# Kernel optimization log

Measured on AMD Instinct MI355X. Metric: run time of the kernel, lower is better.

The kernel has to match this reference:

```python
import jax, jax.numpy as jnp
import numpy as np

WH, WW = 8, 8            # window size
N = WH * WW              # tokens per window = 64
DIM = 512
HEADS = 16
NW = 64                  # windows per image (mask batch)
B = 1024                 # total windows = 16 images * 64 windows
CPB_HIDDEN = 512


def _make_buffers():
    # relative coords table for CPB-MLP: [1, 2*WH-1, 2*WW-1, 2]
    rch = np.arange(-(WH - 1), WH, dtype=np.float32)
    rcw = np.arange(-(WW - 1), WW, dtype=np.float32)
    table = np.stack(np.meshgrid(rch, rcw, indexing='ij'), axis=-1)[None]
    table[..., 0] /= (WH - 1)
    table[..., 1] /= (WW - 1)
    table *= 8.0
    table = np.sign(table) * np.log2(np.abs(table) + 1.0) / 3.0
    # relative position index: [N, N]
    coords = np.stack(np.meshgrid(np.arange(WH), np.arange(WW), indexing='ij'), 0).reshape(2, -1)
    rel = coords[:, :, None] - coords[:, None, :]      # [2, N, N]
    rel = rel.transpose(1, 2, 0).astype(np.int64)
    rel[..., 0] += WH - 1
    rel[..., 1] += WW - 1
    rel[..., 0] *= 2 * WW - 1
    idx = rel.sum(-1)
    return jnp.asarray(table, jnp.float32), jnp.asarray(idx, jnp.int32)


def setup_inputs() -> dict:
    key = jax.random.key(0)
    ks = jax.random.split(key, 8)
    table, idx = _make_buffers()
    return {
        'x': jax.random.normal(ks[0], (B, N, DIM), jnp.float32),
        'mask': jax.random.normal(ks[1], (NW, N, N), jnp.float32),
        'qkv_w': jax.random.normal(ks[2], (3 * DIM, DIM), jnp.float32) * 0.02,
        'q_bias': jnp.zeros((DIM,), jnp.float32),
        'v_bias': jnp.zeros((DIM,), jnp.float32),
        'logit_scale': jnp.full((HEADS, 1, 1), np.log(10.0), jnp.float32),
        'cpb_w1': jax.random.normal(ks[3], (CPB_HIDDEN, 2), jnp.float32) * 0.02,
        'cpb_b1': jnp.zeros((CPB_HIDDEN,), jnp.float32),
        'cpb_w2': jax.random.normal(ks[4], (HEADS, CPB_HIDDEN), jnp.float32) * 0.02,
        'proj_w': jax.random.normal(ks[5], (DIM, DIM), jnp.float32) * 0.02,
        'proj_b': jnp.zeros((DIM,), jnp.float32),
        'rel_coords_table': table,
        'rel_pos_index': idx,
    }


def _l2norm(t):
    n = jnp.sqrt(jnp.sum(t * t, axis=-1, keepdims=True))
    return t / jnp.maximum(n, 1e-12)


def reference(x, mask, qkv_w, q_bias, v_bias, logit_scale, cpb_w1, cpb_b1,
              cpb_w2, proj_w, proj_b, rel_coords_table, rel_pos_index):
    Bq, Nq, C = x.shape
    qkv_b = jnp.concatenate([q_bias, jnp.zeros_like(v_bias), v_bias])
    qkv = x @ qkv_w.T + qkv_b                                  # [B, N, 3C]
    qkv = qkv.reshape(Bq, Nq, 3, HEADS, C // HEADS).transpose(2, 0, 3, 1, 4)
    q, k, v = qkv[0], qkv[1], qkv[2]                           # [B, H, N, D]
    attn = jnp.einsum('bhnd,bhmd->bhnm', _l2norm(q), _l2norm(k))
    scale = jnp.exp(jnp.minimum(logit_scale, jnp.log(jnp.float32(100.0))))
    attn = attn * scale                                        # [B, H, N, N]
    # CPB-MLP relative position bias
    hidden = jax.nn.relu(rel_coords_table @ cpb_w1.T + cpb_b1)  # [1, 2WH-1, 2WW-1, 512]
    bias_table = (hidden @ cpb_w2.T).reshape(-1, HEADS)         # [(2WH-1)(2WW-1), H]
    rel_bias = bias_table[rel_pos_index.reshape(-1)].reshape(Nq, Nq, HEADS)
    rel_bias = 16.0 * jax.nn.sigmoid(rel_bias.transpose(2, 0, 1))  # [H, N, N]
    attn = attn + rel_bias[None]
    nW = mask.shape[0]
    attn = attn.reshape(Bq // nW, nW, HEADS, Nq, Nq) + mask[None, :, None]
    attn = jax.nn.softmax(attn.reshape(Bq, HEADS, Nq, Nq), axis=-1)
    out = jnp.einsum('bhnm,bhmd->bhnd', attn, v)
    out = out.transpose(0, 2, 1, 3).reshape(Bq, Nq, C)
    return out @ proj_w.T + proj_b
```

## Files before the change

### kernel.cpp

```cpp
#include <hip/hip_runtime.h>
#include <hip/hip_bf16.h>

typedef __bf16 bf16;
typedef __bf16 bf16x4 __attribute__((ext_vector_type(4)));
typedef __bf16 bf16x8 __attribute__((ext_vector_type(8)));
typedef float floatx4 __attribute__((ext_vector_type(4)));

#define MFMA16(a, b, c) __builtin_amdgcn_mfma_f32_16x16x32_bf16((a), (b), (c), 0, 0, 0)

static constexpr long OFF_QKV   = 0;
static constexpr long OFF_XB    = 201326592;
static constexpr long OFF_WQKV  = 268435456;
static constexpr long OFF_WPROJ = 270008320;
static constexpr long OFF_BT    = 270532608;
static constexpr long OFF_RB    = 270548992;

__device__ __forceinline__ void load_lds16(const bf16* g, bf16* l) {
  __builtin_amdgcn_global_load_lds((const __attribute__((address_space(1))) void*)(g),
                                   (__attribute__((address_space(3))) void*)(l), 16, 0, 0);
}

__global__ __launch_bounds__(256) void cvt_f32_bf16(const float* __restrict__ src,
                                                    bf16* __restrict__ dst, int n8) {
  int i = blockIdx.x * 256 + threadIdx.x;
  if (i < n8) {
    const float4* s = (const float4*)src;
    float4 a = s[2 * i], b = s[2 * i + 1];
    bf16x8 o;
    o[0] = (bf16)a.x; o[1] = (bf16)a.y; o[2] = (bf16)a.z; o[3] = (bf16)a.w;
    o[4] = (bf16)b.x; o[5] = (bf16)b.y; o[6] = (bf16)b.z; o[7] = (bf16)b.w;
    ((bf16x8*)dst)[i] = o;
  }
}

__global__ __launch_bounds__(256) void cpb_mlp(const float* __restrict__ table,
                                               const float* __restrict__ w1,
                                               const float* __restrict__ b1,
                                               const float* __restrict__ w2,
                                               float* __restrict__ bias_table) {
  __shared__ float hid[512];
  const int e = blockIdx.x;
  const float t0 = table[e * 2 + 0], t1 = table[e * 2 + 1];
  for (int j = threadIdx.x; j < 512; j += 256) {
    float hv = t0 * w1[j * 2 + 0] + t1 * w1[j * 2 + 1] + b1[j];
    hid[j] = hv > 0.f ? hv : 0.f;
  }
  __syncthreads();
  const int hd = threadIdx.x >> 4, l = threadIdx.x & 15;
  float p = 0.f;
  for (int j = l; j < 512; j += 16) p += hid[j] * w2[hd * 512 + j];
  #pragma unroll
  for (int d = 8; d >= 1; d >>= 1) p += __shfl_xor(p, d, 16);
  if (l == 0) bias_table[e * 16 + hd] = p;
}

__global__ __launch_bounds__(256) void cpb_gather(const float* __restrict__ bias_table,
                                                  const int* __restrict__ idx,
                                                  float* __restrict__ rel_bias) {
  int f = blockIdx.x * 256 + threadIdx.x;
  int h = f >> 12, ij = f & 4095;
  float v = bias_table[idx[ij] * 16 + h];
  rel_bias[f] = 16.f / (1.f + __expf(-v));
}

template <int NN, bool QKV>
__global__ __launch_bounds__(512, 2) void gemm_bt(const bf16* __restrict__ A,
                                                  const bf16* __restrict__ Bt,
                                                  void* __restrict__ outv,
                                                  const float* __restrict__ bias_a,
                                                  const float* __restrict__ bias_b) {
  constexpr int K = 512;
  constexpr int nblk = NN / 256;
  __shared__ alignas(16) bf16 As[4][8192];
  __shared__ alignas(16) bf16 Bs[4][8192];
  const int tid = threadIdx.x;
  const int lane = tid & 63;
  const int wv = tid >> 6;
  const int bid = blockIdx.x;
  const int xcd = bid & 7;
  const int g = bid >> 3;
  const int mb = xcd * 32 + g / nblk;
  const int nb = g % nblk;
  const long m0 = (long)mb * 256;
  const int n0 = nb * 256;
  const int wm = (wv >> 2) * 128;
  const int wn = (wv & 3) * 64;
  const int cl = lane & 15;
  const int cq = lane >> 4;
  const int wbase = tid & ~63;
  const int sx = (cq ^ ((cl >> 1) & 3)) << 3;

  const floatx4 fzero = {0.f, 0.f, 0.f, 0.f};
  floatx4 acc[8][4];
  #pragma unroll
  for (int i = 0; i < 8; ++i)
    #pragma unroll
    for (int j = 0; j < 4; ++j) acc[i][j] = fzero;

  auto stageA = [&](int kh) {
    #pragma unroll
    for (int o = 0; o < 2; ++o) {
      const int s = o * 512 + tid;
      const int r = s >> 2;
      const int gl = (s & 3) ^ ((s >> 3) & 3);
      const bf16* ga = A + (m0 + r) * (long)K + kh * 32 + gl * 8;
      load_lds16(ga, &As[kh & 3][(o * 512 + wbase) * 8]);
    }
  };
  auto stageB = [&](int kh) {
    #pragma unroll
    for (int o = 0; o < 2; ++o) {
      const int s = o * 512 + tid;
      const int r = s >> 2;
      const int gl = (s & 3) ^ ((s >> 3) & 3);
      const bf16* gb = Bt + (long)(n0 + r) * K + kh * 32 + gl * 8;
      load_lds16(gb, &Bs[kh & 3][(o * 512 + wbase) * 8]);
    }
  };

  auto kstep = [&](int h, int slot, bool doStage, int vmN, bool lastH) {
    if (doStage) { stageA(h + 3); stageB(h + 3); }
    bf16x8 bfr[4], af[8];
    #pragma unroll
    for (int n = 0; n < 4; ++n) {
      const int r = wn + n * 16 + cl;
      bfr[n] = *(const bf16x8*)&Bs[slot][r * 32 + sx];
    }
    #pragma unroll
    for (int m = 0; m < 8; ++m) {
      const int r = wm + m * 16 + cl;
      af[m] = *(const bf16x8*)&As[slot][r * 32 + sx];
    }
    __builtin_amdgcn_s_setprio(1);
    #pragma unroll
    for (int i = 0; i < 8; ++i)
      #pragma unroll
      for (int j = 0; j < 4; ++j)
        acc[i][j] = MFMA16(bfr[j], af[i], acc[i][j]);
    __builtin_amdgcn_s_setprio(0);
    __builtin_amdgcn_sched_barrier(0);
    if (vmN == 8)      asm volatile("s_waitcnt vmcnt(8)" ::: "memory");
    else if (vmN == 4) asm volatile("s_waitcnt vmcnt(4)" ::: "memory");
    else if (vmN == 0) asm volatile("s_waitcnt vmcnt(0)" ::: "memory");
    if (!lastH) __builtin_amdgcn_s_barrier();
  };

  stageA(0); stageB(0); stageA(1); stageB(1); stageA(2); stageB(2);
  asm volatile("s_waitcnt vmcnt(8)" ::: "memory");
  __builtin_amdgcn_s_barrier();

  #pragma unroll 4
  for (int h = 0; h < 12; ++h) kstep(h, h & 3, true, 8, false);
  kstep(12, 0, true, 8, false);
  kstep(13, 1, false, 4, false);
  kstep(14, 2, false, 0, false);
  kstep(15, 3, false, -1, true);

  const int cq4 = cq * 4;
  #pragma unroll
  for (int i = 0; i < 8; ++i) {
    const long m = m0 + wm + i * 16 + cl;
    #pragma unroll
    for (int j = 0; j < 4; ++j) {
      const int nbase = n0 + wn + j * 16 + cq4;
      if constexpr (QKV) {
        float4 bb = {0.f, 0.f, 0.f, 0.f};
        if (nbase < 512) bb = *(const float4*)&bias_a[nbase];
        else if (nbase >= 1024) bb = *(const float4*)&bias_b[nbase - 1024];
        bf16x4 o;
        o[0] = (bf16)(acc[i][j][0] + bb.x);
        o[1] = (bf16)(acc[i][j][1] + bb.y);
        o[2] = (bf16)(acc[i][j][2] + bb.z);
        o[3] = (bf16)(acc[i][j][3] + bb.w);
        *(bf16x4*)((bf16*)outv + m * NN + nbase) = o;
      } else {
        const float4 bb = *(const float4*)&bias_a[nbase];
        float4 o;
        o.x = acc[i][j][0] + bb.x;
        o.y = acc[i][j][1] + bb.y;
        o.z = acc[i][j][2] + bb.z;
        o.w = acc[i][j][3] + bb.w;
        *(float4*)((float*)outv + m * NN + nbase) = o;
      }
    }
  }
}

__global__ __launch_bounds__(256, 5) void attn_kernel(const bf16* __restrict__ qkv,
                                                      const float* __restrict__ mask,
                                                      const float* __restrict__ lscale,
                                                      const float* __restrict__ rel_bias,
                                                      bf16* __restrict__ out) {
  const int bid = blockIdx.x;
  const int xcd = bid & 7;
  const int t = bid >> 3;
  const int p = xcd + ((t >> 1) << 3);
  const int b = p >> 3;
  const int h = ((p & 7) << 1) | (t & 1);
  const int wi = b & 63;
  const int tid = threadIdx.x;
  const int lane = tid & 63;
  const int wv = tid >> 6;
  const int cl = lane & 15;
  const int cq = lane >> 4;

  __shared__ alignas(16) bf16 smem[12544];
  bf16* qh_s = smem;
  bf16* ql_s = smem + 2560;
  bf16* kh_s = smem + 5120;
  bf16* kl_s = smem + 7680;
  bf16* vT   = smem + 10240;
  bf16* ps   = smem;

  {
    const int r = tid >> 2, seg = tid & 3;
    const bf16* base = qkv + (long)(b * 64 + r) * 1536 + h * 32 + seg * 8;
    float f[8], ss;
    bf16x8 hi, lo;

    bf16x8 qv = *(const bf16x8*)(base);
    ss = 0.f;
    #pragma unroll
    for (int j = 0; j < 8; ++j) { f[j] = (float)qv[j]; ss += f[j] * f[j]; }
    ss += __shfl_xor(ss, 1, 4); ss += __shfl_xor(ss, 2, 4);
    float s1 = 1.f / fmaxf(sqrtf(ss), 1e-12f);
    #pragma unroll
    for (int j = 0; j < 8; ++j) {
      float xn = f[j] * s1;
      bf16 xh = (bf16)xn;
      hi[j] = xh; lo[j] = (bf16)(xn - (float)xh);
    }
    *(bf16x8*)&qh_s[r * 40 + seg * 8] = hi;
    *(bf16x8*)&ql_s[r * 40 + seg * 8] = lo;

    bf16x8 kv = *(const bf16x8*)(base + 512);
    ss = 0.f;
    #pragma unroll
    for (int j = 0; j < 8; ++j) { f[j] = (float)kv[j]; ss += f[j] * f[j]; }
    ss += __shfl_xor(ss, 1, 4); ss += __shfl_xor(ss, 2, 4);
    s1 = 1.f / fmaxf(sqrtf(ss), 1e-12f);
    #pragma unroll
    for (int j = 0; j < 8; ++j) {
      float xn = f[j] * s1;
      bf16 xh = (bf16)xn;
      hi[j] = xh; lo[j] = (bf16)(xn - (float)xh);
    }
    *(bf16x8*)&kh_s[r * 40 + seg * 8] = hi;
    *(bf16x8*)&kl_s[r * 40 + seg * 8] = lo;

    bf16x8 vv = *(const bf16x8*)(base + 1024);
    #pragma unroll
    for (int j = 0; j < 8; ++j) vT[(seg * 8 + j) * 72 + r] = vv[j];
  }
  __syncthreads();

  const float sc = __expf(fminf(lscale[h], 4.6051701859880914f));

  const int mrow = wv * 16 + cl;
  const bf16x8 aqh = *(const bf16x8*)&qh_s[mrow * 40 + cq * 8];
  const bf16x8 aql = *(const bf16x8*)&ql_s[mrow * 40 + cq * 8];
  floatx4 sacc[4];
  #pragma unroll
  for (int nt = 0; nt < 4; ++nt) {
    const int nr = nt * 16 + cl;
    const bf16x8 bkh = *(const bf16x8*)&kh_s[nr * 40 + cq * 8];
    const bf16x8 bkl = *(const bf16x8*)&kl_s[nr * 40 + cq * 8];
    floatx4 a = {0.f, 0.f, 0.f, 0.f};
    a = MFMA16(aql, bkh, a);
    a = MFMA16(aqh, bkl, a);
    a = MFMA16(aqh, bkh, a);
    sacc[nt] = a;
  }
  __syncthreads();

  float pw[4][4];
  #pragma unroll
  for (int rg = 0; rg < 4; ++rg) {
    const int row = wv * 16 + cq * 4 + rg;
    const float* rbp = rel_bias + h * 4096 + row * 64;
    const float* mkp = mask + wi * 4096 + row * 64;
    float mxv = -1e30f;
    #pragma unroll
    for (int nt = 0; nt < 4; ++nt) {
      float s = sacc[nt][rg] * sc + rbp[nt * 16 + cl] + mkp[nt * 16 + cl];
      pw[rg][nt] = s;
      mxv = fmaxf(mxv, s);
    }
    #pragma unroll
    for (int d = 8; d >= 1; d >>= 1) mxv = fmaxf(mxv, __shfl_xor(mxv, d, 16));
    float sm = 0.f;
    #pragma unroll
    for (int nt = 0; nt < 4; ++nt) {
      float e = __expf(pw[rg][nt] - mxv);
      pw[rg][nt] = e;
      sm += e;
    }
    #pragma unroll
    for (int d = 8; d >= 1; d >>= 1) sm += __shfl_xor(sm, d, 16);
    const float inv = 1.f / sm;
    #pragma unroll
    for (int nt = 0; nt < 4; ++nt)
      ps[row * 72 + nt * 16 + cl] = (bf16)(pw[rg][nt] * inv);
  }

  floatx4 oacc[2];
  oacc[0] = (floatx4){0.f, 0.f, 0.f, 0.f};
  oacc[1] = (floatx4){0.f, 0.f, 0.f, 0.f};
  #pragma unroll
  for (int ks = 0; ks < 2; ++ks) {
    const bf16x8 ap = *(const bf16x8*)&ps[(wv * 16 + cl) * 72 + ks * 32 + cq * 8];
    #pragma unroll
    for (int nt = 0; nt < 2; ++nt) {
      const bf16x8 bv = *(const bf16x8*)&vT[(nt * 16 + cl) * 72 + ks * 32 + cq * 8];
      oacc[nt] = MFMA16(bv, ap, oacc[nt]);
    }
  }
  const long obase = (long)(b * 64 + wv * 16 + cl) * 512 + h * 32 + cq * 4;
  #pragma unroll
  for (int nt = 0; nt < 2; ++nt) {
    bf16x4 o;
    #pragma unroll
    for (int r = 0; r < 4; ++r) o[r] = (bf16)oacc[nt][r];
    *(bf16x4*)&out[obase + nt * 16] = o;
  }
}

extern "C" void kernel_launch(void* const* d_in, const int* in_sizes, int n_in,
                              void* d_out, int out_size, void* d_ws, size_t ws_size,
                              hipStream_t stream) {
  const float* x      = (const float*)d_in[0];
  const float* mask   = (const float*)d_in[1];
  const float* qkv_w  = (const float*)d_in[2];
  const float* q_bias = (const float*)d_in[3];
  const float* v_bias = (const float*)d_in[4];
  const float* lsc    = (const float*)d_in[5];
  const float* cpb_w1 = (const float*)d_in[6];
  const float* cpb_b1 = (const float*)d_in[7];
  const float* cpb_w2 = (const float*)d_in[8];
  const float* proj_w = (const float*)d_in[9];
  const float* proj_b = (const float*)d_in[10];
  const float* table  = (const float*)d_in[11];
  const int*   relidx = (const int*)d_in[12];

  char* ws = (char*)d_ws;
  bf16* qkvb   = (bf16*)(ws + OFF_QKV);
  bf16* xb     = (bf16*)(ws + OFF_XB);
  bf16* wqkv   = (bf16*)(ws + OFF_WQKV);
  bf16* wproj  = (bf16*)(ws + OFF_WPROJ);
  float* btab  = (float*)(ws + OFF_BT);
  float* rbias = (float*)(ws + OFF_RB);

  cvt_f32_bf16<<<16384, 256, 0, stream>>>(x, xb, 65536 * 512 / 8);
  cvt_f32_bf16<<<384, 256, 0, stream>>>(qkv_w, wqkv, 1536 * 512 / 8);
  cvt_f32_bf16<<<128, 256, 0, stream>>>(proj_w, wproj, 512 * 512 / 8);
  cpb_mlp<<<225, 256, 0, stream>>>(table, cpb_w1, cpb_b1, cpb_w2, btab);
  cpb_gather<<<256, 256, 0, stream>>>(btab, relidx, rbias);

  gemm_bt<1536, true><<<1536, 512, 0, stream>>>(xb, wqkv, (void*)qkvb, q_bias, v_bias);
  attn_kernel<<<16384, 256, 0, stream>>>(qkvb, mask, lsc, rbias, xb);
  gemm_bt<512, false><<<512, 512, 0, stream>>>(xb, wproj, d_out, proj_b, nullptr);
}
```

Before: 540.1 us.

## Fuse fp32-to-bf16 conversion of x into QKV GEMM A-tile loads

The separate conversion kernel that turned the full fp32 input x into bf16 is removed. The QKV GEMM now loads fp32 A tiles into registers one k-step ahead, converts them to bf16 and writes them to LDS, avoiding the extra full-size write and re-read of the activation buffer. The k-loop for both GEMMs is also restructured into two half-tile MFMA phases with extra barriers, and B staging moves after the first phase. In exchange, the QKV GEMM reads twice as many A bytes per tile, re-read across the N-blocks, and loses asynchronous direct-to-LDS loads for A.

```diff
diff --git a/kernel.cpp b/kernel.cpp
--- a/kernel.cpp
+++ b/kernel.cpp
@@ -64,13 +64,15 @@
 }
 
 template <int NN, bool QKV>
-__global__ __launch_bounds__(512, 2) void gemm_bt(const bf16* __restrict__ A,
+__global__ __launch_bounds__(512, 2) void gemm_bt(const void* __restrict__ Ain,
                                                   const bf16* __restrict__ Bt,
                                                   void* __restrict__ outv,
                                                   const float* __restrict__ bias_a,
                                                   const float* __restrict__ bias_b) {
   constexpr int K = 512;
   constexpr int nblk = NN / 256;
+  const float* Af = (const float*)Ain;
+  const bf16*  Ab = (const bf16*)Ain;
   __shared__ alignas(16) bf16 As[4][8192];
   __shared__ alignas(16) bf16 Bs[4][8192];
   const int tid = threadIdx.x;
@@ -97,64 +99,106 @@
     #pragma unroll
     for (int j = 0; j < 4; ++j) acc[i][j] = fzero;
 
-  auto stageA = [&](int kh) {
-    #pragma unroll
-    for (int o = 0; o < 2; ++o) {
-      const int s = o * 512 + tid;
-      const int r = s >> 2;
-      const int gl = (s & 3) ^ ((s >> 3) & 3);
-      const bf16* ga = A + (m0 + r) * (long)K + kh * 32 + gl * 8;
-      load_lds16(ga, &As[kh & 3][(o * 512 + wbase) * 8]);
-    }
+  const int rp0 = tid >> 2;
+  const int rp1 = rp0 + 128;
+  const int gl0 = (tid & 3) ^ ((tid >> 3) & 3);
+
+  auto stageB = [&](int j) {
+    const bf16* gb0 = Bt + (long)(n0 + rp0) * K + j * 32 + gl0 * 8;
+    load_lds16(gb0, &Bs[j & 3][wbase * 8]);
+    const bf16* gb1 = Bt + (long)(n0 + rp1) * K + j * 32 + gl0 * 8;
+    load_lds16(gb1, &Bs[j & 3][(512 + wbase) * 8]);
   };
-  auto stageB = [&](int kh) {
-    #pragma unroll
-    for (int o = 0; o < 2; ++o) {
-      const int s = o * 512 + tid;
-      const int r = s >> 2;
-      const int gl = (s & 3) ^ ((s >> 3) & 3);
-      const bf16* gb = Bt + (long)(n0 + r) * K + kh * 32 + gl * 8;
-      load_lds16(gb, &Bs[kh & 3][(o * 512 + wbase) * 8]);
-    }
+  auto stageA_gl = [&](int j) {
+    const bf16* ga0 = Ab + (m0 + rp0) * (long)K + j * 32 + gl0 * 8;
+    load_lds16(ga0, &As[j & 3][wbase * 8]);
+    const bf16* ga1 = Ab + (m0 + rp1) * (long)K + j * 32 + gl0 * 8;
+    load_lds16(ga1, &As[j & 3][(512 + wbase) * 8]);
   };
 
-  auto kstep = [&](int h, int slot, bool doStage, int vmN, bool lastH) {
-    if (doStage) { stageA(h + 3); stageB(h + 3); }
-    bf16x8 bfr[4], af[8];
-    #pragma unroll
-    for (int n = 0; n < 4; ++n) {
-      const int r = wn + n * 16 + cl;
-      bfr[n] = *(const bf16x8*)&Bs[slot][r * 32 + sx];
-    }
-    #pragma unroll
-    for (int m = 0; m < 8; ++m) {
-      const int r = wm + m * 16 + cl;
-      af[m] = *(const bf16x8*)&As[slot][r * 32 + sx];
-    }
+  float4 a0, a1, a2, a3;
+  auto issueA = [&](int j) {
+    const float4* s0 = (const float4*)(Af + (m0 + rp0) * (long)K + j * 32 + gl0 * 8);
+    const float4* s1 = (const float4*)(Af + (m0 + rp1) * (long)K + j * 32 + gl0 * 8);
+    a0 = s0[0]; a1 = s0[1]; a2 = s1[0]; a3 = s1[1];
+  };
+  auto writeA = [&](int j) {
+    bf16x8 v0, v1;
+    v0[0] = (bf16)a0.x; v0[1] = (bf16)a0.y; v0[2] = (bf16)a0.z; v0[3] = (bf16)a0.w;
+    v0[4] = (bf16)a1.x; v0[5] = (bf16)a1.y; v0[6] = (bf16)a1.z; v0[7] = (bf16)a1.w;
+    v1[0] = (bf16)a2.x; v1[1] = (bf16)a2.y; v1[2] = (bf16)a2.z; v1[3] = (bf16)a2.w;
+    v1[4] = (bf16)a3.x; v1[5] = (bf16)a3.y; v1[6] = (bf16)a3.z; v1[7] = (bf16)a3.w;
+    *(bf16x8*)&As[j & 3][tid * 8] = v0;
+    *(bf16x8*)&As[j & 3][(512 + tid) * 8] = v1;
+  };
+
+  if constexpr (QKV) {
+    issueA(0);
+    stageB(0); stageB(1); stageB(2);
+    writeA(0);
+    asm volatile("s_waitcnt vmcnt(4)" ::: "memory");
+    asm volatile("s_waitcnt lgkmcnt(0)" ::: "memory");
+  } else {
+    stageA_gl(0); stageB(0); stageA_gl(1); stageB(1); stageA_gl(2); stageB(2);
+    asm volatile("s_waitcnt vmcnt(8)" ::: "memory");
+  }
+  __builtin_amdgcn_s_barrier();
+
+  #pragma unroll
+  for (int h = 0; h < 16; ++h) {
+    const int slot = h & 3;
+    if constexpr (QKV) {
+      if (h + 1 <= 15) issueA(h + 1);
+    } else {
+      if (h + 3 <= 15) stageA_gl(h + 3);
+    }
+    bf16x8 af0[4], bfr[4];
+    #pragma unroll
+    for (int m = 0; m < 4; ++m)
+      af0[m] = *(const bf16x8*)&As[slot][(wm + m * 16 + cl) * 32 + sx];
+    #pragma unroll
+    for (int n = 0; n < 4; ++n)
+      bfr[n] = *(const bf16x8*)&Bs[slot][(wn + n * 16 + cl) * 32 + sx];
+    __builtin_amdgcn_s_barrier();
+    asm volatile("s_waitcnt lgkmcnt(0)" ::: "memory");
+    __builtin_amdgcn_sched_barrier(0);
     __builtin_amdgcn_s_setprio(1);
     #pragma unroll
-    for (int i = 0; i < 8; ++i)
+    for (int i = 0; i < 4; ++i)
       #pragma unroll
       for (int j = 0; j < 4; ++j)
-        acc[i][j] = MFMA16(bfr[j], af[i], acc[i][j]);
+        acc[i][j] = MFMA16(bfr[j], af0[i], acc[i][j]);
     __builtin_amdgcn_s_setprio(0);
+    __builtin_amdgcn_s_barrier();
     __builtin_amdgcn_sched_barrier(0);
-    if (vmN == 8)      asm volatile("s_waitcnt vmcnt(8)" ::: "memory");
-    else if (vmN == 4) asm volatile("s_waitcnt vmcnt(4)" ::: "memory");
-    else if (vmN == 0) asm volatile("s_waitcnt vmcnt(0)" ::: "memory");
-    if (!lastH) __builtin_amdgcn_s_barrier();
-  };
-
-  stageA(0); stageB(0); stageA(1); stageB(1); stageA(2); stageB(2);
-  asm volatile("s_waitcnt vmcnt(8)" ::: "memory");
-  __builtin_amdgcn_s_barrier();
-
-  #pragma unroll 4
-  for (int h = 0; h < 12; ++h) kstep(h, h & 3, true, 8, false);
-  kstep(12, 0, true, 8, false);
-  kstep(13, 1, false, 4, false);
-  kstep(14, 2, false, 0, false);
-  kstep(15, 3, false, -1, true);
+    if (h + 3 <= 15) stageB(h + 3);
+    if constexpr (QKV) {
+      if (h <= 12) asm volatile("s_waitcnt vmcnt(2)" ::: "memory");
+      if (h + 1 <= 15) writeA(h + 1);
+    } else {
+      if (h <= 12)      asm volatile("s_waitcnt vmcnt(8)" ::: "memory");
+      else if (h == 13) asm volatile("s_waitcnt vmcnt(4)" ::: "memory");
+      else if (h == 14) asm volatile("s_waitcnt vmcnt(0)" ::: "memory");
+    }
+    bf16x8 af1[4];
+    #pragma unroll
+    for (int m = 0; m < 4; ++m)
+      af1[m] = *(const bf16x8*)&As[slot][(wm + 64 + m * 16 + cl) * 32 + sx];
+    asm volatile("s_waitcnt lgkmcnt(0)" ::: "memory");
+    __builtin_amdgcn_s_barrier();
+    __builtin_amdgcn_sched_barrier(0);
+    __builtin_amdgcn_s_setprio(1);
+    #pragma unroll
+    for (int i = 0; i < 4; ++i)
+      #pragma unroll
+      for (int j = 0; j < 4; ++j)
+        acc[4 + i][j] = MFMA16(bfr[j], af1[i], acc[4 + i][j]);
+    __builtin_amdgcn_s_setprio(0);
+    if (h < 15) {
+      __builtin_amdgcn_s_barrier();
+      __builtin_amdgcn_sched_barrier(0);
+    }
+  }
 
   const int cq4 = cq * 4;
   #pragma unroll
@@ -350,13 +394,14 @@
   float* btab  = (float*)(ws + OFF_BT);
   float* rbias = (float*)(ws + OFF_RB);
 
-  cvt_f32_bf16<<<16384, 256, 0, stream>>>(x, xb, 65536 * 512 / 8);
   cvt_f32_bf16<<<384, 256, 0, stream>>>(qkv_w, wqkv, 1536 * 512 / 8);
   cvt_f32_bf16<<<128, 256, 0, stream>>>(proj_w, wproj, 512 * 512 / 8);
   cpb_mlp<<<225, 256, 0, stream>>>(table, cpb_w1, cpb_b1, cpb_w2, btab);
   cpb_gather<<<256, 256, 0, stream>>>(btab, relidx, rbias);
 
-  gemm_bt<1536, true><<<1536, 512, 0, stream>>>(xb, wqkv, (void*)qkvb, q_bias, v_bias);
+  gemm_bt<1536, true><<<1536, 512, 0, stream>>>((const void*)x, wqkv, (void*)qkvb,
+                                                q_bias, v_bias);
   attn_kernel<<<16384, 256, 0, stream>>>(qkvb, mask, lsc, rbias, xb);
-  gemm_bt<512, false><<<512, 512, 0, stream>>>(xb, wproj, d_out, proj_b, nullptr);
-}
+  gemm_bt<512, false><<<512, 512, 0, stream>>>((const void*)xb, wproj, d_out,
+                                               proj_b, nullptr);
+}
```

New measurement: 587.6 us. 1.09x slower.

## Add smaller-tile projection GEMM and transpose attention score MFMA for vectorized softmax

Applied to the files above, without the earlier changes.

The output projection gets its own kernel with 128x128 tiles, 256 threads, and a 3-slot LDS pipeline. This launches 2048 blocks instead of 512 so more CUs stay busy on the small N=512 GEMM. In attention, the QK^T MFMA operands are swapped so each lane holds one query row's scores. The softmax can then load bias and mask as float4, reduce with two cross-lane shuffles instead of four per row, and write probabilities as bf16x4. The smaller tiles lower data reuse per block.

```diff
diff --git a/kernel.cpp b/kernel.cpp
--- a/kernel.cpp
+++ b/kernel.cpp
@@ -63,13 +63,13 @@
   rel_bias[f] = 16.f / (1.f + __expf(-v));
 }
 
-template <int NN, bool QKV>
-__global__ __launch_bounds__(512, 2) void gemm_bt(const bf16* __restrict__ A,
-                                                  const bf16* __restrict__ Bt,
-                                                  void* __restrict__ outv,
-                                                  const float* __restrict__ bias_a,
-                                                  const float* __restrict__ bias_b) {
+__global__ __launch_bounds__(512, 2) void gemm_qkv(const bf16* __restrict__ A,
+                                                   const bf16* __restrict__ Bt,
+                                                   bf16* __restrict__ out,
+                                                   const float* __restrict__ bias_a,
+                                                   const float* __restrict__ bias_b) {
   constexpr int K = 512;
+  constexpr int NN = 1536;
   constexpr int nblk = NN / 256;
   __shared__ alignas(16) bf16 As[4][8192];
   __shared__ alignas(16) bf16 Bs[4][8192];
@@ -122,15 +122,11 @@
     if (doStage) { stageA(h + 3); stageB(h + 3); }
     bf16x8 bfr[4], af[8];
     #pragma unroll
-    for (int n = 0; n < 4; ++n) {
-      const int r = wn + n * 16 + cl;
-      bfr[n] = *(const bf16x8*)&Bs[slot][r * 32 + sx];
-    }
-    #pragma unroll
-    for (int m = 0; m < 8; ++m) {
-      const int r = wm + m * 16 + cl;
-      af[m] = *(const bf16x8*)&As[slot][r * 32 + sx];
-    }
+    for (int n = 0; n < 4; ++n)
+      bfr[n] = *(const bf16x8*)&Bs[slot][(wn + n * 16 + cl) * 32 + sx];
+    #pragma unroll
+    for (int m = 0; m < 8; ++m)
+      af[m] = *(const bf16x8*)&As[slot][(wm + m * 16 + cl) * 32 + sx];
     __builtin_amdgcn_s_setprio(1);
     #pragma unroll
     for (int i = 0; i < 8; ++i)
@@ -163,25 +159,115 @@
     #pragma unroll
     for (int j = 0; j < 4; ++j) {
       const int nbase = n0 + wn + j * 16 + cq4;
-      if constexpr (QKV) {
-        float4 bb = {0.f, 0.f, 0.f, 0.f};
-        if (nbase < 512) bb = *(const float4*)&bias_a[nbase];
-        else if (nbase >= 1024) bb = *(const float4*)&bias_b[nbase - 1024];
-        bf16x4 o;
-        o[0] = (bf16)(acc[i][j][0] + bb.x);
-        o[1] = (bf16)(acc[i][j][1] + bb.y);
-        o[2] = (bf16)(acc[i][j][2] + bb.z);
-        o[3] = (bf16)(acc[i][j][3] + bb.w);
-        *(bf16x4*)((bf16*)outv + m * NN + nbase) = o;
-      } else {
-        const float4 bb = *(const float4*)&bias_a[nbase];
-        float4 o;
-        o.x = acc[i][j][0] + bb.x;
-        o.y = acc[i][j][1] + bb.y;
-        o.z = acc[i][j][2] + bb.z;
-        o.w = acc[i][j][3] + bb.w;
-        *(float4*)((float*)outv + m * NN + nbase) = o;
-      }
+      float4 bb = {0.f, 0.f, 0.f, 0.f};
+      if (nbase < 512) bb = *(const float4*)&bias_a[nbase];
+      else if (nbase >= 1024) bb = *(const float4*)&bias_b[nbase - 1024];
+      bf16x4 o;
+      o[0] = (bf16)(acc[i][j][0] + bb.x);
+      o[1] = (bf16)(acc[i][j][1] + bb.y);
+      o[2] = (bf16)(acc[i][j][2] + bb.z);
+      o[3] = (bf16)(acc[i][j][3] + bb.w);
+      *(bf16x4*)(out + m * NN + nbase) = o;
+    }
+  }
+}
+
+__global__ __launch_bounds__(256, 4) void gemm_proj(const bf16* __restrict__ A,
+                                                    const bf16* __restrict__ Bt,
+                                                    float* __restrict__ outv,
+                                                    const float* __restrict__ bias_a) {
+  constexpr int K = 512;
+  constexpr int KT = K / 32;
+  constexpr int NN = 512;
+  constexpr int nblk = NN / 128;
+  __shared__ alignas(16) bf16 As[3][128 * 32];
+  __shared__ alignas(16) bf16 Bs[3][128 * 32];
+  const int tid = threadIdx.x;
+  const int lane = tid & 63;
+  const int wv = tid >> 6;
+  const int bid = blockIdx.x;
+  const int xcd = bid & 7;
+  const int g = bid >> 3;
+  const int mb = xcd * 64 + g / nblk;
+  const int nb = g % nblk;
+  const long m0 = (long)mb * 128;
+  const int n0 = nb * 128;
+  const int wm = (wv & 1) * 64;
+  const int wn = (wv >> 1) * 64;
+  const int cl = lane & 15;
+  const int cq = lane >> 4;
+  const int wbase = tid & ~63;
+
+  const floatx4 fzero = {0.f, 0.f, 0.f, 0.f};
+  floatx4 acc[4][4];
+  #pragma unroll
+  for (int i = 0; i < 4; ++i)
+    #pragma unroll
+    for (int j = 0; j < 4; ++j) acc[i][j] = fzero;
+
+  int srow[2], sgl[2];
+  #pragma unroll
+  for (int r = 0; r < 2; ++r) {
+    const int s = r * 256 + tid;
+    srow[r] = s >> 2;
+    sgl[r] = (s & 3) ^ ((s >> 3) & 3);
+  }
+  const int sx = cq ^ ((cl >> 1) & 3);
+
+  auto stage = [&](int slot, int j) {
+    const int k0 = j * 32;
+    #pragma unroll
+    for (int r = 0; r < 2; ++r) {
+      const bf16* ga = A + (m0 + srow[r]) * (long)K + (k0 + sgl[r] * 8);
+      load_lds16(ga, &As[slot][(r * 256 + wbase) * 8]);
+      const bf16* gb = Bt + (long)(n0 + srow[r]) * K + (k0 + sgl[r] * 8);
+      load_lds16(gb, &Bs[slot][(r * 256 + wbase) * 8]);
+    }
+  };
+
+  stage(0, 0);
+  stage(1, 1);
+  asm volatile("s_waitcnt vmcnt(4)" ::: "memory");
+  __builtin_amdgcn_s_barrier();
+
+  #pragma unroll
+  for (int h = 0; h < KT; ++h) {
+    const int slot = h % 3;
+    if (h + 2 < KT) stage((h + 2) % 3, h + 2);
+    bf16x8 af[4], bfr[4];
+    #pragma unroll
+    for (int t = 0; t < 4; ++t) {
+      af[t] = *(const bf16x8*)&As[slot][((wm + t * 16 + cl) * 4 + sx) * 8];
+      bfr[t] = *(const bf16x8*)&Bs[slot][((wn + t * 16 + cl) * 4 + sx) * 8];
+    }
+    __builtin_amdgcn_s_setprio(1);
+    #pragma unroll
+    for (int i = 0; i < 4; ++i)
+      #pragma unroll
+      for (int j = 0; j < 4; ++j)
+        acc[i][j] = MFMA16(bfr[j], af[i], acc[i][j]);
+    __builtin_amdgcn_s_setprio(0);
+    if (h <= KT - 3)
+      asm volatile("s_waitcnt vmcnt(4)" ::: "memory");
+    else if (h == KT - 2)
+      asm volatile("s_waitcnt vmcnt(0)" ::: "memory");
+    if (h + 1 < KT) __builtin_amdgcn_s_barrier();
+  }
+
+  const int cq4 = cq * 4;
+  #pragma unroll
+  for (int i = 0; i < 4; ++i) {
+    const long m = m0 + wm + i * 16 + cl;
+    #pragma unroll
+    for (int j = 0; j < 4; ++j) {
+      const int nbase = n0 + wn + j * 16 + cq4;
+      const float4 bb = *(const float4*)&bias_a[nbase];
+      float4 o;
+      o.x = acc[i][j][0] + bb.x;
+      o.y = acc[i][j][1] + bb.y;
+      o.z = acc[i][j][2] + bb.z;
+      o.w = acc[i][j][3] + bb.w;
+      *(float4*)(outv + m * NN + nbase) = o;
     }
   }
 }
@@ -256,9 +342,9 @@
 
   const float sc = __expf(fminf(lscale[h], 4.6051701859880914f));
 
-  const int mrow = wv * 16 + cl;
-  const bf16x8 aqh = *(const bf16x8*)&qh_s[mrow * 40 + cq * 8];
-  const bf16x8 aql = *(const bf16x8*)&ql_s[mrow * 40 + cq * 8];
+  const int row = wv * 16 + cl;
+  const bf16x8 aqh = *(const bf16x8*)&qh_s[row * 40 + cq * 8];
+  const bf16x8 aql = *(const bf16x8*)&ql_s[row * 40 + cq * 8];
   floatx4 sacc[4];
   #pragma unroll
   for (int nt = 0; nt < 4; ++nt) {
@@ -266,41 +352,52 @@
     const bf16x8 bkh = *(const bf16x8*)&kh_s[nr * 40 + cq * 8];
     const bf16x8 bkl = *(const bf16x8*)&kl_s[nr * 40 + cq * 8];
     floatx4 a = {0.f, 0.f, 0.f, 0.f};
-    a = MFMA16(aql, bkh, a);
-    a = MFMA16(aqh, bkl, a);
-    a = MFMA16(aqh, bkh, a);
+    a = MFMA16(bkh, aql, a);
+    a = MFMA16(bkl, aqh, a);
+    a = MFMA16(bkh, aqh, a);
     sacc[nt] = a;
   }
+
+  const float* rbp = rel_bias + h * 4096 + row * 64 + cq * 4;
+  const float* mkp = mask + wi * 4096 + row * 64 + cq * 4;
+  floatx4 rbv[4], mkv[4];
+  #pragma unroll
+  for (int nt = 0; nt < 4; ++nt) {
+    rbv[nt] = *(const floatx4*)&rbp[nt * 16];
+    mkv[nt] = *(const floatx4*)&mkp[nt * 16];
+  }
   __syncthreads();
 
   float pw[4][4];
-  #pragma unroll
-  for (int rg = 0; rg < 4; ++rg) {
-    const int row = wv * 16 + cq * 4 + rg;
-    const float* rbp = rel_bias + h * 4096 + row * 64;
-    const float* mkp = mask + wi * 4096 + row * 64;
-    float mxv = -1e30f;
-    #pragma unroll
-    for (int nt = 0; nt < 4; ++nt) {
-      float s = sacc[nt][rg] * sc + rbp[nt * 16 + cl] + mkp[nt * 16 + cl];
-      pw[rg][nt] = s;
+  float mxv = -1e30f;
+  #pragma unroll
+  for (int nt = 0; nt < 4; ++nt)
+    #pragma unroll
+    for (int r = 0; r < 4; ++r) {
+      float s = sacc[nt][r] * sc + rbv[nt][r] + mkv[nt][r];
+      pw[nt][r] = s;
       mxv = fmaxf(mxv, s);
     }
-    #pragma unroll
-    for (int d = 8; d >= 1; d >>= 1) mxv = fmaxf(mxv, __shfl_xor(mxv, d, 16));
-    float sm = 0.f;
-    #pragma unroll
-    for (int nt = 0; nt < 4; ++nt) {
-      float e = __expf(pw[rg][nt] - mxv);
-      pw[rg][nt] = e;
+  mxv = fmaxf(mxv, __shfl_xor(mxv, 16));
+  mxv = fmaxf(mxv, __shfl_xor(mxv, 32));
+  float sm = 0.f;
+  #pragma unroll
+  for (int nt = 0; nt < 4; ++nt)
+    #pragma unroll
+    for (int r = 0; r < 4; ++r) {
+      float e = __expf(pw[nt][r] - mxv);
+      pw[nt][r] = e;
       sm += e;
     }
-    #pragma unroll
-    for (int d = 8; d >= 1; d >>= 1) sm += __shfl_xor(sm, d, 16);
-    const float inv = 1.f / sm;
-    #pragma unroll
-    for (int nt = 0; nt < 4; ++nt)
-      ps[row * 72 + nt * 16 + cl] = (bf16)(pw[rg][nt] * inv);
+  sm += __shfl_xor(sm, 16);
+  sm += __shfl_xor(sm, 32);
+  const float inv = 1.f / sm;
+  #pragma unroll
+  for (int nt = 0; nt < 4; ++nt) {
+    bf16x4 o;
+    #pragma unroll
+    for (int r = 0; r < 4; ++r) o[r] = (bf16)(pw[nt][r] * inv);
+    *(bf16x4*)&ps[row * 72 + nt * 16 + cq * 4] = o;
   }
 
   floatx4 oacc[2];
@@ -308,14 +405,14 @@
   oacc[1] = (floatx4){0.f, 0.f, 0.f, 0.f};
   #pragma unroll
   for (int ks = 0; ks < 2; ++ks) {
-    const bf16x8 ap = *(const bf16x8*)&ps[(wv * 16 + cl) * 72 + ks * 32 + cq * 8];
+    const bf16x8 ap = *(const bf16x8*)&ps[row * 72 + ks * 32 + cq * 8];
     #pragma unroll
     for (int nt = 0; nt < 2; ++nt) {
       const bf16x8 bv = *(const bf16x8*)&vT[(nt * 16 + cl) * 72 + ks * 32 + cq * 8];
       oacc[nt] = MFMA16(bv, ap, oacc[nt]);
     }
   }
-  const long obase = (long)(b * 64 + wv * 16 + cl) * 512 + h * 32 + cq * 4;
+  const long obase = (long)(b * 64 + row) * 512 + h * 32 + cq * 4;
   #pragma unroll
   for (int nt = 0; nt < 2; ++nt) {
     bf16x4 o;
@@ -356,7 +453,7 @@
   cpb_mlp<<<225, 256, 0, stream>>>(table, cpb_w1, cpb_b1, cpb_w2, btab);
   cpb_gather<<<256, 256, 0, stream>>>(btab, relidx, rbias);
 
-  gemm_bt<1536, true><<<1536, 512, 0, stream>>>(xb, wqkv, (void*)qkvb, q_bias, v_bias);
+  gemm_qkv<<<1536, 512, 0, stream>>>(xb, wqkv, qkvb, q_bias, v_bias);
   attn_kernel<<<16384, 256, 0, stream>>>(qkvb, mask, lsc, rbias, xb);
-  gemm_bt<512, false><<<512, 512, 0, stream>>>(xb, wproj, d_out, proj_b, nullptr);
-}
+  gemm_proj<<<2048, 256, 0, stream>>>(xb, wproj, (float*)d_out, proj_b);
+}
```

After: 561.5 us. 1.04x slower.

## Fuse fp32-to-bf16 conversion of x into the QKV GEMM A-tile load

Applied to the files above, without the earlier changes.

Drops the standalone kernel that converted the 128 MB fp32 input x to bf16. The QKV GEMM now reads fp32 x directly through registers, converts it to bf16 and writes it into LDS, using a 2-stage double buffer instead of the previous 4-stage async global-to-LDS pipeline. This removes a full write and reread of the bf16 copy. In exchange, each GEMM tile rereads the fp32 A data (six N-blocks per row block, twice the bytes of bf16), and the shallower pipeline with register staging may expose more latency.

```diff
diff --git a/kernel.cpp b/kernel.cpp
--- a/kernel.cpp
+++ b/kernel.cpp
@@ -63,13 +63,128 @@
   rel_bias[f] = 16.f / (1.f + __expf(-v));
 }
 
-template <int NN, bool QKV>
-__global__ __launch_bounds__(512, 2) void gemm_bt(const bf16* __restrict__ A,
-                                                  const bf16* __restrict__ Bt,
-                                                  void* __restrict__ outv,
-                                                  const float* __restrict__ bias_a,
-                                                  const float* __restrict__ bias_b) {
+__global__ __launch_bounds__(512, 2) void gemm_qkv(const float* __restrict__ Af,
+                                                   const bf16* __restrict__ Bt,
+                                                   bf16* __restrict__ out,
+                                                   const float* __restrict__ bias_a,
+                                                   const float* __restrict__ bias_b) {
   constexpr int K = 512;
+  constexpr int NN = 1536;
+  __shared__ alignas(16) bf16 As[2][8192];
+  __shared__ alignas(16) bf16 Bs[2][8192];
+  const int tid = threadIdx.x;
+  const int lane = tid & 63;
+  const int wv = tid >> 6;
+  const int bid = blockIdx.x;
+  const int xcd = bid & 7;
+  const int g = bid >> 3;
+  const int mb = xcd * 32 + g / 6;
+  const int nb = g % 6;
+  const long m0 = (long)mb * 256;
+  const int n0 = nb * 256;
+  const int wm = (wv >> 2) * 128;
+  const int wn = (wv & 3) * 64;
+  const int cl = lane & 15;
+  const int cq = lane >> 4;
+  const int wbase = tid & ~63;
+  const int sx = (cq ^ ((cl >> 1) & 3)) << 3;
+
+  const floatx4 fzero = {0.f, 0.f, 0.f, 0.f};
+  floatx4 acc[8][4];
+  #pragma unroll
+  for (int i = 0; i < 8; ++i)
+    #pragma unroll
+    for (int j = 0; j < 4; ++j) acc[i][j] = fzero;
+
+  const int rp0 = tid >> 2;
+  const int gl0 = (tid & 3) ^ ((tid >> 3) & 3);
+
+  auto stageB = [&](int j) {
+    const bf16* gb0 = Bt + (long)(n0 + rp0) * K + j * 32 + gl0 * 8;
+    load_lds16(gb0, &Bs[j & 1][wbase * 8]);
+    const bf16* gb1 = Bt + (long)(n0 + rp0 + 128) * K + j * 32 + gl0 * 8;
+    load_lds16(gb1, &Bs[j & 1][(512 + wbase) * 8]);
+  };
+
+  float4 fa0, fa1, fa2, fa3;
+  auto issueA = [&](int j) {
+    const float* s0 = Af + (m0 + rp0) * (long)K + j * 32 + gl0 * 8;
+    fa0 = ((const float4*)s0)[0];
+    fa1 = ((const float4*)s0)[1];
+    const float* s1 = Af + (m0 + rp0 + 128) * (long)K + j * 32 + gl0 * 8;
+    fa2 = ((const float4*)s1)[0];
+    fa3 = ((const float4*)s1)[1];
+  };
+  auto writeA = [&](int j) {
+    bf16x8 v0, v1;
+    v0[0] = (bf16)fa0.x; v0[1] = (bf16)fa0.y; v0[2] = (bf16)fa0.z; v0[3] = (bf16)fa0.w;
+    v0[4] = (bf16)fa1.x; v0[5] = (bf16)fa1.y; v0[6] = (bf16)fa1.z; v0[7] = (bf16)fa1.w;
+    v1[0] = (bf16)fa2.x; v1[1] = (bf16)fa2.y; v1[2] = (bf16)fa2.z; v1[3] = (bf16)fa2.w;
+    v1[4] = (bf16)fa3.x; v1[5] = (bf16)fa3.y; v1[6] = (bf16)fa3.z; v1[7] = (bf16)fa3.w;
+    *(bf16x8*)&As[j & 1][tid * 8] = v0;
+    *(bf16x8*)&As[j & 1][(512 + tid) * 8] = v1;
+  };
+
+  issueA(0);
+  stageB(0);
+  writeA(0);
+  asm volatile("s_waitcnt vmcnt(0)" ::: "memory");
+  asm volatile("s_waitcnt lgkmcnt(0)" ::: "memory");
+  __builtin_amdgcn_s_barrier();
+
+  #pragma unroll
+  for (int h = 0; h < 16; ++h) {
+    const int slot = h & 1;
+    if (h + 1 < 16) { stageB(h + 1); issueA(h + 1); }
+    bf16x8 bfr[4], af[8];
+    #pragma unroll
+    for (int n = 0; n < 4; ++n)
+      bfr[n] = *(const bf16x8*)&Bs[slot][(wn + n * 16 + cl) * 32 + sx];
+    #pragma unroll
+    for (int m = 0; m < 8; ++m)
+      af[m] = *(const bf16x8*)&As[slot][(wm + m * 16 + cl) * 32 + sx];
+    __builtin_amdgcn_s_setprio(1);
+    #pragma unroll
+    for (int i = 0; i < 8; ++i)
+      #pragma unroll
+      for (int j = 0; j < 4; ++j)
+        acc[i][j] = MFMA16(bfr[j], af[i], acc[i][j]);
+    __builtin_amdgcn_s_setprio(0);
+    __builtin_amdgcn_sched_barrier(0);
+    if (h + 1 < 16) {
+      asm volatile("s_waitcnt vmcnt(4)" ::: "memory");
+      writeA(h + 1);
+      asm volatile("s_waitcnt lgkmcnt(0)" ::: "memory");
+      __builtin_amdgcn_s_barrier();
+    }
+  }
+
+  const int cq4 = cq * 4;
+  #pragma unroll
+  for (int i = 0; i < 8; ++i) {
+    const long m = m0 + wm + i * 16 + cl;
+    #pragma unroll
+    for (int j = 0; j < 4; ++j) {
+      const int nbase = n0 + wn + j * 16 + cq4;
+      float4 bb = {0.f, 0.f, 0.f, 0.f};
+      if (nbase < 512) bb = *(const float4*)&bias_a[nbase];
+      else if (nbase >= 1024) bb = *(const float4*)&bias_b[nbase - 1024];
+      bf16x4 o;
+      o[0] = (bf16)(acc[i][j][0] + bb.x);
+      o[1] = (bf16)(acc[i][j][1] + bb.y);
+      o[2] = (bf16)(acc[i][j][2] + bb.z);
+      o[3] = (bf16)(acc[i][j][3] + bb.w);
+      *(bf16x4*)(out + m * NN + nbase) = o;
+    }
+  }
+}
+
+__global__ __launch_bounds__(512, 2) void gemm_proj(const bf16* __restrict__ A,
+                                                    const bf16* __restrict__ Bt,
+                                                    float* __restrict__ outv,
+                                                    const float* __restrict__ bias_a) {
+  constexpr int K = 512;
+  constexpr int NN = 512;
   constexpr int nblk = NN / 256;
   __shared__ alignas(16) bf16 As[4][8192];
   __shared__ alignas(16) bf16 Bs[4][8192];
@@ -122,15 +237,11 @@
     if (doStage) { stageA(h + 3); stageB(h + 3); }
     bf16x8 bfr[4], af[8];
     #pragma unroll
-    for (int n = 0; n < 4; ++n) {
-      const int r = wn + n * 16 + cl;
-      bfr[n] = *(const bf16x8*)&Bs[slot][r * 32 + sx];
-    }
-    #pragma unroll
-    for (int m = 0; m < 8; ++m) {
-      const int r = wm + m * 16 + cl;
-      af[m] = *(const bf16x8*)&As[slot][r * 32 + sx];
-    }
+    for (int n = 0; n < 4; ++n)
+      bfr[n] = *(const bf16x8*)&Bs[slot][(wn + n * 16 + cl) * 32 + sx];
+    #pragma unroll
+    for (int m = 0; m < 8; ++m)
+      af[m] = *(const bf16x8*)&As[slot][(wm + m * 16 + cl) * 32 + sx];
     __builtin_amdgcn_s_setprio(1);
     #pragma unroll
     for (int i = 0; i < 8; ++i)
@@ -163,25 +274,13 @@
     #pragma unroll
     for (int j = 0; j < 4; ++j) {
       const int nbase = n0 + wn + j * 16 + cq4;
-      if constexpr (QKV) {
-        float4 bb = {0.f, 0.f, 0.f, 0.f};
-        if (nbase < 512) bb = *(const float4*)&bias_a[nbase];
-        else if (nbase >= 1024) bb = *(const float4*)&bias_b[nbase - 1024];
-        bf16x4 o;
-        o[0] = (bf16)(acc[i][j][0] + bb.x);
-        o[1] = (bf16)(acc[i][j][1] + bb.y);
-        o[2] = (bf16)(acc[i][j][2] + bb.z);
-        o[3] = (bf16)(acc[i][j][3] + bb.w);
-        *(bf16x4*)((bf16*)outv + m * NN + nbase) = o;
-      } else {
-        const float4 bb = *(const float4*)&bias_a[nbase];
-        float4 o;
-        o.x = acc[i][j][0] + bb.x;
-        o.y = acc[i][j][1] + bb.y;
-        o.z = acc[i][j][2] + bb.z;
-        o.w = acc[i][j][3] + bb.w;
-        *(float4*)((float*)outv + m * NN + nbase) = o;
-      }
+      const float4 bb = *(const float4*)&bias_a[nbase];
+      float4 o;
+      o.x = acc[i][j][0] + bb.x;
+      o.y = acc[i][j][1] + bb.y;
+      o.z = acc[i][j][2] + bb.z;
+      o.w = acc[i][j][3] + bb.w;
+      *(float4*)(outv + m * NN + nbase) = o;
     }
   }
 }
@@ -350,13 +449,12 @@
   float* btab  = (float*)(ws + OFF_BT);
   float* rbias = (float*)(ws + OFF_RB);
 
-  cvt_f32_bf16<<<16384, 256, 0, stream>>>(x, xb, 65536 * 512 / 8);
   cvt_f32_bf16<<<384, 256, 0, stream>>>(qkv_w, wqkv, 1536 * 512 / 8);
   cvt_f32_bf16<<<128, 256, 0, stream>>>(proj_w, wproj, 512 * 512 / 8);
   cpb_mlp<<<225, 256, 0, stream>>>(table, cpb_w1, cpb_b1, cpb_w2, btab);
   cpb_gather<<<256, 256, 0, stream>>>(btab, relidx, rbias);
 
-  gemm_bt<1536, true><<<1536, 512, 0, stream>>>(xb, wqkv, (void*)qkvb, q_bias, v_bias);
+  gemm_qkv<<<1536, 512, 0, stream>>>(x, wqkv, qkvb, q_bias, v_bias);
   attn_kernel<<<16384, 256, 0, stream>>>(qkvb, mask, lsc, rbias, xb);
-  gemm_bt<512, false><<<512, 512, 0, stream>>>(xb, wproj, d_out, proj_b, nullptr);
-}
+  gemm_proj<<<512, 512, 0, stream>>>(xb, wproj, (float*)d_out, proj_b);
+}
```

Result: slower. 594.1 us (+10.0%).
